# Kernel optimization log

Hardware: AMD Instinct MI355X
Metric: run time of the kernel (lower is better)

The kernel has to match this reference:

```python
import jax, jax.numpy as jnp
import numpy as np

B, Z, L = 256, 256, 8
C0, H0, W0 = 128, 8, 8
O = C0 * H0 * W0  # 8192


def _conv_transpose(x, w, b):
    """Torch ConvTranspose2d(k=4, s=2, p=1) equivalent.
    w: torch layout (in_ch, out_ch, kH, kW).
    Implemented as lhs-dilated conv with flipped, transposed kernel; pad = k-1-p = 2.
    """
    wt = jnp.flip(w, (2, 3)).transpose(1, 0, 2, 3)  # (out, in, kh, kw)
    y = jax.lax.conv_general_dilated(
        x, wt, window_strides=(1, 1), padding=[(2, 2), (2, 2)],
        lhs_dilation=(2, 2), dimension_numbers=('NCHW', 'OIHW', 'NCHW'))
    return y + b[None, :, None, None]


def setup_inputs() -> dict:
    key = jax.random.key(0)
    ks = jax.random.split(key, 6)
    return {
        'x': jax.random.normal(ks[0], (B, Z), jnp.float32),
        'gw': jax.random.normal(ks[1], (Z, L), jnp.float32) * (2.0 / (Z + L)) ** 0.5,  # xavier_normal
        'gb': jnp.zeros((L,), jnp.float32),
        'pw': jax.random.normal(ks[2], (O, Z, L), jnp.float32) * (1.0 / Z) ** 0.5,  # kaiming linear
        'pb': jnp.zeros((O, L), jnp.float32),
        'w1': jax.random.normal(ks[3], (C0, 64, 4, 4), jnp.float32) * 0.02,
        'b1': jnp.zeros((64,), jnp.float32),
        'w2': jax.random.normal(ks[4], (64, 32, 4, 4), jnp.float32) * 0.02,
        'b2': jnp.zeros((32,), jnp.float32),
        'w3': jax.random.normal(ks[5], (32, 3, 4, 4), jnp.float32) * 0.02,
        'b3': jnp.zeros((3,), jnp.float32),
    }


def reference(x, gw, gb, pw, pb, w1, b1, w2, b2, w3, b3):
    # --- ME mixture of linear experts (linear projection) ---
    g = jax.nn.softmax(x @ gw + gb, axis=1)               # (B, L)
    # Per-expert linear outputs, then gate-weighted sum. Mathematically equal to
    # torch's (pw @ gatings) per-sample weight followed by bmm with x, but avoids
    # the (B, O, Z) intermediate.
    expert_out = jnp.einsum('bi,oil->bol', x, pw)          # (B, O, L)
    out = jnp.einsum('bol,bl->bo', expert_out, g) + g @ pb.T  # (B, O)
    # --- conv-transpose decoder stack ---
    h = out.reshape(B, C0, H0, W0)
    h = jax.nn.relu(_conv_transpose(h, w1, b1))            # (B, 64, 16, 16)
    h = jax.nn.relu(_conv_transpose(h, w2, b2))            # (B, 32, 32, 32)
    h = _conv_transpose(h, w3, b3)                         # (B, 3, 64, 64)
    return h
```

## Files before the change

kernel.cpp:

```cpp
#include <hip/hip_runtime.h>

typedef __bf16 bf16;
typedef __bf16 bf16x8 __attribute__((ext_vector_type(8)));
typedef float f32x4 __attribute__((ext_vector_type(4)));

__device__ __forceinline__ f32x4 mfma16(bf16x8 a, bf16x8 b, f32x4 c) {
  return __builtin_amdgcn_mfma_f32_16x16x32_bf16(a, b, c, 0, 0, 0);
}

__device__ __forceinline__ void gload16(const void* g, void* l) {
  __builtin_amdgcn_global_load_lds(
      (const __attribute__((address_space(1))) void*)g,
      (__attribute__((address_space(3))) void*)(uint32_t)(size_t)l, 16, 0, 0);
}

__device__ __forceinline__ bf16x8 cvt8(float4 a, float4 b) {
  bf16x8 r;
  r[0] = (bf16)a.x; r[1] = (bf16)a.y; r[2] = (bf16)a.z; r[3] = (bf16)a.w;
  r[4] = (bf16)b.x; r[5] = (bf16)b.y; r[6] = (bf16)b.z; r[7] = (bf16)b.w;
  return r;
}

__global__ __launch_bounds__(256) void gating_kernel(
    const float* __restrict__ x, const float* __restrict__ gw,
    const float* __restrict__ gb, bf16* __restrict__ xgbP,
    float* __restrict__ gbuf) {
  const int b = blockIdx.x, tid = threadIdx.x;
  __shared__ float xs[256];
  __shared__ float gs[8];
  xs[tid] = x[b * 256 + tid];
  __syncthreads();
  if (tid < 8) {
    float acc = gb[tid];
    for (int i = 0; i < 256; ++i) acc += xs[i] * gw[i * 8 + tid];
    gs[tid] = acc;
  }
  __syncthreads();
  if (tid == 0) {
    float m = gs[0];
    for (int l = 1; l < 8; ++l) m = fmaxf(m, gs[l]);
    float s = 0.f, e[8];
    for (int l = 0; l < 8; ++l) { e[l] = expf(gs[l] - m); s += e[l]; }
    float inv = 1.f / s;
    for (int l = 0; l < 8; ++l) gs[l] = e[l] * inv;
  }
  __syncthreads();
  if (tid < 8) gbuf[b * 8 + tid] = gs[tid];
  float xv = xs[tid];
  bf16x8 r;
#pragma unroll
  for (int j = 0; j < 8; ++j) r[j] = (bf16)(xv * gs[j]);
  size_t off = (size_t)(b >> 4) * 65536 + (size_t)(tid >> 2) * 1024 +
               (size_t)(((tid & 3) * 16 + (b & 15)) * 16);
  *(bf16x8*)((char*)xgbP + off) = r;
}

template <int CIN, int COUT, int COUTP>
__device__ __forceinline__ void cw_one(const float* __restrict__ w,
                                       bf16* __restrict__ wp, int idx) {
  constexpr int K = 4 * CIN;
  int ic = idx & (CIN - 1);
  int t = (idx / CIN) & 3;
  int oc = (idx / K) % COUTP;
  int p = idx / (K * COUTP);
  bf16 v = (bf16)0.f;
  if (oc < COUT) {
    int py = p >> 1, px = p & 1, tyi = t >> 1, txi = t & 1;
    int ky = py == 0 ? (tyi ? 3 : 1) : (tyi ? 2 : 0);
    int kx = px == 0 ? (txi ? 3 : 1) : (txi ? 2 : 0);
    v = (bf16)w[((ic * COUT + oc) * 4 + ky) * 4 + kx];
  }
  wp[idx] = v;
}

__global__ __launch_bounds__(256) void convert_w_all(
    const float* __restrict__ w1, bf16* __restrict__ w1p,
    const float* __restrict__ w2, bf16* __restrict__ w2p,
    const float* __restrict__ w3, bf16* __restrict__ w3p) {
  int idx = blockIdx.x * 256 + threadIdx.x;
  if (idx < 131072) cw_one<128, 64, 64>(w1, w1p, idx);
  else if (idx < 163840) cw_one<64, 32, 32>(w2, w2p, idx - 131072);
  else if (idx < 172032) cw_one<32, 3, 16>(w3, w3p, idx - 163840);
}

template <int HP, int WP, int C>
__device__ __forceinline__ void bz_one(bf16* __restrict__ buf, int idx) {
  constexpr int NCELL = 2 * WP + 2 * (HP - 2);
  constexpr int C8 = C / 8;
  int c8 = idx % C8;
  int rem = idx / C8;
  int cell = rem % NCELL;
  int b = rem / NCELL;
  int y, x;
  if (cell < WP) { y = 0; x = cell; }
  else if (cell < 2 * WP) { y = HP - 1; x = cell - WP; }
  else { int r2 = cell - 2 * WP; y = 1 + (r2 >> 1); x = (r2 & 1) ? WP - 1 : 0; }
  bf16x8 z = {};
  *(bf16x8*)(buf + ((size_t)(b * HP + y) * WP + x) * C + c8 * 8) = z;
}

__global__ __launch_bounds__(256) void border_zero_all(
    bf16* __restrict__ h0t, bf16* __restrict__ h1, bf16* __restrict__ h2) {
  int idx = blockIdx.x * 256 + threadIdx.x;
  if (idx < 147456) bz_one<10, 10, 128>(h0t, idx);
  else if (idx < 286720) bz_one<18, 18, 64>(h1, idx - 147456);
  else if (idx < 421888) bz_one<34, 34, 32>(h2, idx - 286720);
}

__global__ __launch_bounds__(512) void me_gemm_kernel(
    const float* __restrict__ pw, const bf16* __restrict__ xgbP,
    const float* __restrict__ pb, const float* __restrict__ gbuf,
    bf16* __restrict__ h0t) {
  __shared__ char sA[131072];
  const int tid = threadIdx.x, wv = tid >> 6, l = tid & 63;
  const int lr = l & 15, lkg = l >> 4;
  const int M0 = blockIdx.x * 32;

#pragma unroll 4
  for (int it = 0; it < 16; ++it) {
    int g = it * 512 + tid;
    int kt = g >> 8, rem = g & 255;
    int row = rem >> 3, ig = rem & 7;
    const float* src = pw + (size_t)(M0 + row) * 2048 + kt * 64 + ig * 8;
    float4 v0 = *(const float4*)src;
    float4 v1 = *(const float4*)(src + 4);
    int L = kt * 4096 + row * 128 + ((ig * 16) ^ ((row & 7) << 4));
    *(bf16x8*)(sA + L) = cvt8(v0, v1);
  }
  __syncthreads();

  int aoff[2][2];
#pragma unroll
  for (int m = 0; m < 2; ++m)
#pragma unroll
    for (int ks = 0; ks < 2; ++ks)
      aoff[m][ks] = (m * 16 + lr) * 128 + (((ks * 4 + lkg) * 16) ^ ((lr & 7) << 4));

  const char* pB0 = (const char*)xgbP + (size_t)(2 * wv) * 65536 + l * 16;
  const char* pB1 = (const char*)xgbP + (size_t)(2 * wv + 1) * 65536 + l * 16;

  f32x4 acc[2][2] = {};
#pragma unroll 8
  for (int s = 0; s < 64; ++s) {
    const int kt = s >> 1, ks = s & 1;
    const char* base = sA + kt * 4096;
    bf16x8 a0 = *(const bf16x8*)(base + aoff[0][ks]);
    bf16x8 a1 = *(const bf16x8*)(base + aoff[1][ks]);
    bf16x8 b0 = *(const bf16x8*)(pB0 + s * 1024);
    bf16x8 b1 = *(const bf16x8*)(pB1 + s * 1024);
    acc[0][0] = mfma16(a0, b0, acc[0][0]);
    acc[0][1] = mfma16(a0, b1, acc[0][1]);
    acc[1][0] = mfma16(a1, b0, acc[1][0]);
    acc[1][1] = mfma16(a1, b1, acc[1][1]);
  }

  float4 g0[2], g1[2];
#pragma unroll
  for (int n = 0; n < 2; ++n) {
    int b = wv * 32 + n * 16 + lr;
    g0[n] = *(const float4*)(gbuf + b * 8);
    g1[n] = *(const float4*)(gbuf + b * 8 + 4);
  }
#pragma unroll
  for (int m = 0; m < 2; ++m)
#pragma unroll
    for (int r = 0; r < 4; ++r) {
      int o = M0 + m * 16 + lkg * 4 + r;
      float4 p0 = *(const float4*)(pb + o * 8);
      float4 p1 = *(const float4*)(pb + o * 8 + 4);
      int cch = o >> 6, y = (o >> 3) & 7, xx = o & 7;
#pragma unroll
      for (int n = 0; n < 2; ++n) {
        int b = wv * 32 + n * 16 + lr;
        float bias = g0[n].x * p0.x + g0[n].y * p0.y + g0[n].z * p0.z + g0[n].w * p0.w +
                     g1[n].x * p1.x + g1[n].y * p1.y + g1[n].z * p1.z + g1[n].w * p1.w;
        h0t[((size_t)(b * 10 + y + 1) * 10 + xx + 1) * 128 + cch] = (bf16)(acc[m][n][r] + bias);
      }
    }
}

template <int CIN, int H, int YB, int COUTP, int WM, int NF, int SWM,
          bool WLDS, int INIT, int WIT, bool RELU, bool F32OUT, int SIN_SZ, int SW_SZ>
__global__ __launch_bounds__(256) void convt_kernel(
    const bf16* __restrict__ in, const bf16* __restrict__ wp,
    const float* __restrict__ bias, bf16* __restrict__ out,
    float* __restrict__ fout) {
  constexpr int W = H, WROW = W + 2, ROWB = CIN * 2, GRS = ROWB / 16;
  constexpr int LGR = (GRS == 16) ? 4 : (GRS == 8) ? 3 : 2;
  constexpr int LW = (W == 8) ? 3 : (W == 16) ? 4 : 5;
  constexpr int K = 4 * CIN;
  constexpr int CHUNKS = (YB + 2) * WROW * GRS;
  constexpr int WGR = K / 8;
  __shared__ char sIn[SIN_SZ];
  __shared__ char sW[SW_SZ];

  const int tid = threadIdx.x, wv = tid >> 6, l = tid & 63;
  const int nyb = H / YB;
  const int img = blockIdx.x / nyb, y0 = (blockIdx.x % nyb) * YB;
  const int p = blockIdx.y, py = p >> 1, px = p & 1;

#pragma unroll
  for (int it = 0; it < INIT; ++it) {
    int t = it * 256 + tid;
    int tc = t < CHUNKS ? t : CHUNKS - 1;
    int pix = tc >> LGR, cc = tc & (GRS - 1);
    int ly = pix / WROW, lx = pix % WROW;
    int sb = (cc * 16) ^ ((pix & SWM) << 4);
    gload16(in + ((size_t)((img * (H + 2) + y0 + ly) * (W + 2) + lx)) * CIN + (sb >> 1),
            sIn + it * 4096 + wv * 1024);
  }
  if constexpr (WLDS) {
#pragma unroll
    for (int it = 0; it < WIT; ++it) {
      int t = it * 256 + tid;
      int oc = t / WGR, cc = t % WGR;
      int sb = (cc * 16) ^ ((oc & 7) << 4);
      gload16(wp + (size_t)(p * COUTP + oc) * K + (sb >> 1), sW + it * 4096 + wv * 1024);
    }
  }
  __syncthreads();

  const int lr = l & 15, lkg = l >> 4;
  const int wm = wv & (WM - 1), wn = wv / WM;
  int pcen[2];
#pragma unroll
  for (int m = 0; m < 2; ++m) {
    int r = wm * 32 + m * 16 + lr;
    pcen[m] = ((r >> LW) + 1) * WROW + (r & (W - 1)) + 1;
  }

  f32x4 acc[2][NF] = {};
#pragma unroll 4
  for (int kk = 0; kk < K; kk += 32) {
    const int t4 = kk / CIN;
    const int tyi = t4 >> 1, txi = t4 & 1;
    const int dy = (py == 0) ? (tyi ? -1 : 0) : (tyi ? 0 : 1);
    const int dx = (px == 0) ? (txi ? -1 : 0) : (txi ? 0 : 1);
    const int icb = (kk % CIN) * 2 + lkg * 16;
    bf16x8 av[2], bv[NF];
#pragma unroll
    for (int m = 0; m < 2; ++m) {
      int pixd = pcen[m] + dy * WROW + dx;
      av[m] = *(const bf16x8*)(sIn + pixd * ROWB + (icb ^ ((pixd & SWM) << 4)));
    }
#pragma unroll
    for (int n = 0; n < NF; ++n) {
      int oc = (wn * NF + n) * 16 + lr;
      if constexpr (WLDS) {
        int kb = kk * 2 + lkg * 16;
        bv[n] = *(const bf16x8*)(sW + oc * (K * 2) + (kb ^ ((oc & 7) << 4)));
      } else {
        bv[n] = *(const bf16x8*)(wp + (size_t)(p * COUTP + oc) * K + kk + lkg * 8);
      }
    }
#pragma unroll
    for (int m = 0; m < 2; ++m)
#pragma unroll
      for (int n = 0; n < NF; ++n) acc[m][n] = mfma16(av[m], bv[n], acc[m][n]);
  }

#pragma unroll
  for (int m = 0; m < 2; ++m)
#pragma unroll
    for (int r4 = 0; r4 < 4; ++r4) {
      int r = wm * 32 + m * 16 + lkg * 4 + r4;
      int yy = r >> LW, xx = r & (W - 1);
      int oy = 2 * (y0 + yy) + py, ox = 2 * xx + px;
#pragma unroll
      for (int n = 0; n < NF; ++n) {
        int oc = (wn * NF + n) * 16 + lr;
        float v = acc[m][n][r4];
        if constexpr (F32OUT) {
          if (oc < 3) fout[((size_t)(img * 3 + oc) * (2 * H) + oy) * (2 * H) + ox] = v + bias[oc];
        } else {
          v += bias[oc];
          if constexpr (RELU) v = fmaxf(v, 0.f);
          out[((size_t)(img * (2 * H + 2) + oy + 1) * (2 * H + 2) + ox + 1) * COUTP + oc] = (bf16)v;
        }
      }
    }
}

extern "C" void kernel_launch(void* const* d_in, const int* in_sizes, int n_in,
                              void* d_out, int out_size, void* d_ws, size_t ws_size,
                              hipStream_t stream) {
  const float* x  = (const float*)d_in[0];
  const float* gw = (const float*)d_in[1];
  const float* gb = (const float*)d_in[2];
  const float* pw = (const float*)d_in[3];
  const float* pb = (const float*)d_in[4];
  const float* w1 = (const float*)d_in[5];
  const float* b1 = (const float*)d_in[6];
  const float* w2 = (const float*)d_in[7];
  const float* b2 = (const float*)d_in[8];
  const float* w3 = (const float*)d_in[9];
  const float* b3 = (const float*)d_in[10];
  float* outp = (float*)d_out;

  char* ws = (char*)d_ws;
  bf16*  xgbP = (bf16*)(ws + 0);
  float* gbuf = (float*)(ws + 1048576);
  bf16*  h0t  = (bf16*)(ws + 1056768);
  bf16*  w1p  = (bf16*)(ws + 7610368);
  bf16*  h1   = (bf16*)(ws + 7872512);
  bf16*  w2p  = (bf16*)(ws + 18489344);
  bf16*  h2   = (bf16*)(ws + 18554880);
  bf16*  w3p  = (bf16*)(ws + 37494784);

  border_zero_all<<<1648, 256, 0, stream>>>(h0t, h1, h2);
  gating_kernel<<<256, 256, 0, stream>>>(x, gw, gb, xgbP, gbuf);
  convert_w_all<<<672, 256, 0, stream>>>(w1, w1p, w2, w2p, w3, w3p);

  me_gemm_kernel<<<256, 512, 0, stream>>>(pw, xgbP, pb, gbuf, h0t);

  convt_kernel<128, 8, 8, 64, 2, 2, 7, false, 7, 0, true, false, 28672, 16>
      <<<dim3(256, 4), 256, 0, stream>>>(h0t, w1p, b1, h1, nullptr);
  convt_kernel<64, 16, 8, 32, 4, 2, 7, true, 6, 4, true, false, 24576, 16384>
      <<<dim3(512, 4), 256, 0, stream>>>(h1, w2p, b2, h2, nullptr);
  convt_kernel<32, 32, 4, 16, 4, 1, 3, true, 4, 1, false, true, 16384, 4096>
      <<<dim3(2048, 4), 256, 0, stream>>>(h2, w3p, b3, nullptr, outp);
}
```

Measured before the change: 115.6 us.

## Fold four conv-transpose parities into one block and halve ME GEMM tile

Each conv-transpose block now loops over all four output parity classes itself, so the staged input tile in LDS is loaded once and reused four times instead of being reloaded by four separate grid-y blocks. Weight staging in LDS is dropped and weights are read straight from global memory. Separately, the ME GEMM tile shrinks from 32 to 16 rows, halving LDS use and doubling the block count. The trade-offs are four times the accumulator registers per thread, a quarter of the conv blocks, and more global weight traffic.

```diff
diff --git a/kernel.cpp b/kernel.cpp
--- a/kernel.cpp
+++ b/kernel.cpp
@@ -111,47 +111,42 @@
     const float* __restrict__ pw, const bf16* __restrict__ xgbP,
     const float* __restrict__ pb, const float* __restrict__ gbuf,
     bf16* __restrict__ h0t) {
-  __shared__ char sA[131072];
+  __shared__ char sA[65536];
   const int tid = threadIdx.x, wv = tid >> 6, l = tid & 63;
   const int lr = l & 15, lkg = l >> 4;
-  const int M0 = blockIdx.x * 32;
-
-#pragma unroll 4
-  for (int it = 0; it < 16; ++it) {
+  const int M0 = blockIdx.x * 16;
+
+#pragma unroll
+  for (int it = 0; it < 8; ++it) {
     int g = it * 512 + tid;
-    int kt = g >> 8, rem = g & 255;
+    int kt = g >> 7, rem = g & 127;
     int row = rem >> 3, ig = rem & 7;
     const float* src = pw + (size_t)(M0 + row) * 2048 + kt * 64 + ig * 8;
     float4 v0 = *(const float4*)src;
     float4 v1 = *(const float4*)(src + 4);
-    int L = kt * 4096 + row * 128 + ((ig * 16) ^ ((row & 7) << 4));
+    int L = kt * 2048 + row * 128 + ((ig * 16) ^ ((row & 7) << 4));
     *(bf16x8*)(sA + L) = cvt8(v0, v1);
   }
   __syncthreads();
 
-  int aoff[2][2];
-#pragma unroll
-  for (int m = 0; m < 2; ++m)
-#pragma unroll
-    for (int ks = 0; ks < 2; ++ks)
-      aoff[m][ks] = (m * 16 + lr) * 128 + (((ks * 4 + lkg) * 16) ^ ((lr & 7) << 4));
+  int aoff[2];
+#pragma unroll
+  for (int ks = 0; ks < 2; ++ks)
+    aoff[ks] = lr * 128 + (((ks * 4 + lkg) * 16) ^ ((lr & 7) << 4));
 
   const char* pB0 = (const char*)xgbP + (size_t)(2 * wv) * 65536 + l * 16;
   const char* pB1 = (const char*)xgbP + (size_t)(2 * wv + 1) * 65536 + l * 16;
 
-  f32x4 acc[2][2] = {};
+  f32x4 acc[2] = {};
 #pragma unroll 8
   for (int s = 0; s < 64; ++s) {
     const int kt = s >> 1, ks = s & 1;
-    const char* base = sA + kt * 4096;
-    bf16x8 a0 = *(const bf16x8*)(base + aoff[0][ks]);
-    bf16x8 a1 = *(const bf16x8*)(base + aoff[1][ks]);
+    const char* base = sA + kt * 2048;
+    bf16x8 a0 = *(const bf16x8*)(base + aoff[ks]);
     bf16x8 b0 = *(const bf16x8*)(pB0 + s * 1024);
     bf16x8 b1 = *(const bf16x8*)(pB1 + s * 1024);
-    acc[0][0] = mfma16(a0, b0, acc[0][0]);
-    acc[0][1] = mfma16(a0, b1, acc[0][1]);
-    acc[1][0] = mfma16(a1, b0, acc[1][0]);
-    acc[1][1] = mfma16(a1, b1, acc[1][1]);
+    acc[0] = mfma16(a0, b0, acc[0]);
+    acc[1] = mfma16(a0, b1, acc[1]);
   }
 
   float4 g0[2], g1[2];
@@ -162,25 +157,23 @@
     g1[n] = *(const float4*)(gbuf + b * 8 + 4);
   }
 #pragma unroll
-  for (int m = 0; m < 2; ++m)
-#pragma unroll
-    for (int r = 0; r < 4; ++r) {
-      int o = M0 + m * 16 + lkg * 4 + r;
-      float4 p0 = *(const float4*)(pb + o * 8);
-      float4 p1 = *(const float4*)(pb + o * 8 + 4);
-      int cch = o >> 6, y = (o >> 3) & 7, xx = o & 7;
-#pragma unroll
-      for (int n = 0; n < 2; ++n) {
-        int b = wv * 32 + n * 16 + lr;
-        float bias = g0[n].x * p0.x + g0[n].y * p0.y + g0[n].z * p0.z + g0[n].w * p0.w +
-                     g1[n].x * p1.x + g1[n].y * p1.y + g1[n].z * p1.z + g1[n].w * p1.w;
-        h0t[((size_t)(b * 10 + y + 1) * 10 + xx + 1) * 128 + cch] = (bf16)(acc[m][n][r] + bias);
-      }
+  for (int r = 0; r < 4; ++r) {
+    int o = M0 + lkg * 4 + r;
+    float4 p0 = *(const float4*)(pb + o * 8);
+    float4 p1 = *(const float4*)(pb + o * 8 + 4);
+    int cch = o >> 6, y = (o >> 3) & 7, xx = o & 7;
+#pragma unroll
+    for (int n = 0; n < 2; ++n) {
+      int b = wv * 32 + n * 16 + lr;
+      float bias = g0[n].x * p0.x + g0[n].y * p0.y + g0[n].z * p0.z + g0[n].w * p0.w +
+                   g1[n].x * p1.x + g1[n].y * p1.y + g1[n].z * p1.z + g1[n].w * p1.w;
+      h0t[((size_t)(b * 10 + y + 1) * 10 + xx + 1) * 128 + cch] = (bf16)(acc[n][r] + bias);
     }
-}
-
-template <int CIN, int H, int YB, int COUTP, int WM, int NF, int SWM,
-          bool WLDS, int INIT, int WIT, bool RELU, bool F32OUT, int SIN_SZ, int SW_SZ>
+  }
+}
+
+template <int CIN, int H, int YB, int COUTP, int WM, int NF, int SWM, int INIT,
+          bool RELU, bool F32OUT, int SIN_SZ>
 __global__ __launch_bounds__(256) void convt_kernel(
     const bf16* __restrict__ in, const bf16* __restrict__ wp,
     const float* __restrict__ bias, bf16* __restrict__ out,
@@ -190,14 +183,11 @@
   constexpr int LW = (W == 8) ? 3 : (W == 16) ? 4 : 5;
   constexpr int K = 4 * CIN;
   constexpr int CHUNKS = (YB + 2) * WROW * GRS;
-  constexpr int WGR = K / 8;
   __shared__ char sIn[SIN_SZ];
-  __shared__ char sW[SW_SZ];
 
   const int tid = threadIdx.x, wv = tid >> 6, l = tid & 63;
   const int nyb = H / YB;
   const int img = blockIdx.x / nyb, y0 = (blockIdx.x % nyb) * YB;
-  const int p = blockIdx.y, py = p >> 1, px = p & 1;
 
 #pragma unroll
   for (int it = 0; it < INIT; ++it) {
@@ -209,15 +199,6 @@
     gload16(in + ((size_t)((img * (H + 2) + y0 + ly) * (W + 2) + lx)) * CIN + (sb >> 1),
             sIn + it * 4096 + wv * 1024);
   }
-  if constexpr (WLDS) {
-#pragma unroll
-    for (int it = 0; it < WIT; ++it) {
-      int t = it * 256 + tid;
-      int oc = t / WGR, cc = t % WGR;
-      int sb = (cc * 16) ^ ((oc & 7) << 4);
-      gload16(wp + (size_t)(p * COUTP + oc) * K + (sb >> 1), sW + it * 4096 + wv * 1024);
-    }
-  }
   __syncthreads();
 
   const int lr = l & 15, lkg = l >> 4;
@@ -229,56 +210,59 @@
     pcen[m] = ((r >> LW) + 1) * WROW + (r & (W - 1)) + 1;
   }
 
-  f32x4 acc[2][NF] = {};
+  f32x4 acc[4][2][NF] = {};
+#pragma unroll
+  for (int p = 0; p < 4; ++p) {
+    const int py = p >> 1, px = p & 1;
 #pragma unroll 4
-  for (int kk = 0; kk < K; kk += 32) {
-    const int t4 = kk / CIN;
-    const int tyi = t4 >> 1, txi = t4 & 1;
-    const int dy = (py == 0) ? (tyi ? -1 : 0) : (tyi ? 0 : 1);
-    const int dx = (px == 0) ? (txi ? -1 : 0) : (txi ? 0 : 1);
-    const int icb = (kk % CIN) * 2 + lkg * 16;
-    bf16x8 av[2], bv[NF];
-#pragma unroll
-    for (int m = 0; m < 2; ++m) {
-      int pixd = pcen[m] + dy * WROW + dx;
-      av[m] = *(const bf16x8*)(sIn + pixd * ROWB + (icb ^ ((pixd & SWM) << 4)));
-    }
-#pragma unroll
-    for (int n = 0; n < NF; ++n) {
-      int oc = (wn * NF + n) * 16 + lr;
-      if constexpr (WLDS) {
-        int kb = kk * 2 + lkg * 16;
-        bv[n] = *(const bf16x8*)(sW + oc * (K * 2) + (kb ^ ((oc & 7) << 4)));
-      } else {
+    for (int kk = 0; kk < K; kk += 32) {
+      const int t4 = kk / CIN;
+      const int tyi = t4 >> 1, txi = t4 & 1;
+      const int dy = (py == 0) ? (tyi ? -1 : 0) : (tyi ? 0 : 1);
+      const int dx = (px == 0) ? (txi ? -1 : 0) : (txi ? 0 : 1);
+      const int icb = (kk % CIN) * 2 + lkg * 16;
+      bf16x8 av[2], bv[NF];
+#pragma unroll
+      for (int m = 0; m < 2; ++m) {
+        int pixd = pcen[m] + dy * WROW + dx;
+        av[m] = *(const bf16x8*)(sIn + pixd * ROWB + (icb ^ ((pixd & SWM) << 4)));
+      }
+#pragma unroll
+      for (int n = 0; n < NF; ++n) {
+        int oc = (wn * NF + n) * 16 + lr;
         bv[n] = *(const bf16x8*)(wp + (size_t)(p * COUTP + oc) * K + kk + lkg * 8);
       }
+#pragma unroll
+      for (int m = 0; m < 2; ++m)
+#pragma unroll
+        for (int n = 0; n < NF; ++n) acc[p][m][n] = mfma16(av[m], bv[n], acc[p][m][n]);
     }
+  }
+
+#pragma unroll
+  for (int p = 0; p < 4; ++p) {
+    const int py = p >> 1, px = p & 1;
 #pragma unroll
     for (int m = 0; m < 2; ++m)
 #pragma unroll
-      for (int n = 0; n < NF; ++n) acc[m][n] = mfma16(av[m], bv[n], acc[m][n]);
-  }
-
-#pragma unroll
-  for (int m = 0; m < 2; ++m)
-#pragma unroll
-    for (int r4 = 0; r4 < 4; ++r4) {
-      int r = wm * 32 + m * 16 + lkg * 4 + r4;
-      int yy = r >> LW, xx = r & (W - 1);
-      int oy = 2 * (y0 + yy) + py, ox = 2 * xx + px;
-#pragma unroll
-      for (int n = 0; n < NF; ++n) {
-        int oc = (wn * NF + n) * 16 + lr;
-        float v = acc[m][n][r4];
-        if constexpr (F32OUT) {
-          if (oc < 3) fout[((size_t)(img * 3 + oc) * (2 * H) + oy) * (2 * H) + ox] = v + bias[oc];
-        } else {
-          v += bias[oc];
-          if constexpr (RELU) v = fmaxf(v, 0.f);
-          out[((size_t)(img * (2 * H + 2) + oy + 1) * (2 * H + 2) + ox + 1) * COUTP + oc] = (bf16)v;
+      for (int r4 = 0; r4 < 4; ++r4) {
+        int r = wm * 32 + m * 16 + lkg * 4 + r4;
+        int yy = r >> LW, xx = r & (W - 1);
+        int oy = 2 * (y0 + yy) + py, ox = 2 * xx + px;
+#pragma unroll
+        for (int n = 0; n < NF; ++n) {
+          int oc = (wn * NF + n) * 16 + lr;
+          float v = acc[p][m][n][r4];
+          if constexpr (F32OUT) {
+            if (oc < 3) fout[((size_t)(img * 3 + oc) * (2 * H) + oy) * (2 * H) + ox] = v + bias[oc];
+          } else {
+            v += bias[oc];
+            if constexpr (RELU) v = fmaxf(v, 0.f);
+            out[((size_t)(img * (2 * H + 2) + oy + 1) * (2 * H + 2) + ox + 1) * COUTP + oc] = (bf16)v;
+          }
         }
       }
-    }
+  }
 }
 
 extern "C" void kernel_launch(void* const* d_in, const int* in_sizes, int n_in,
@@ -311,12 +295,12 @@
   gating_kernel<<<256, 256, 0, stream>>>(x, gw, gb, xgbP, gbuf);
   convert_w_all<<<672, 256, 0, stream>>>(w1, w1p, w2, w2p, w3, w3p);
 
-  me_gemm_kernel<<<256, 512, 0, stream>>>(pw, xgbP, pb, gbuf, h0t);
-
-  convt_kernel<128, 8, 8, 64, 2, 2, 7, false, 7, 0, true, false, 28672, 16>
-      <<<dim3(256, 4), 256, 0, stream>>>(h0t, w1p, b1, h1, nullptr);
-  convt_kernel<64, 16, 8, 32, 4, 2, 7, true, 6, 4, true, false, 24576, 16384>
-      <<<dim3(512, 4), 256, 0, stream>>>(h1, w2p, b2, h2, nullptr);
-  convt_kernel<32, 32, 4, 16, 4, 1, 3, true, 4, 1, false, true, 16384, 4096>
-      <<<dim3(2048, 4), 256, 0, stream>>>(h2, w3p, b3, nullptr, outp);
-}
+  me_gemm_kernel<<<512, 512, 0, stream>>>(pw, xgbP, pb, gbuf, h0t);
+
+  convt_kernel<128, 8, 8, 64, 2, 2, 7, 7, true, false, 28672>
+      <<<256, 256, 0, stream>>>(h0t, w1p, b1, h1, nullptr);
+  convt_kernel<64, 16, 8, 32, 4, 2, 7, 6, true, false, 24576>
+      <<<512, 256, 0, stream>>>(h1, w2p, b2, h2, nullptr);
+  convt_kernel<32, 32, 4, 16, 4, 1, 3, 4, false, true, 16384>
+      <<<2048, 256, 0, stream>>>(h2, w3p, b3, nullptr, outp);
+}
```

After: 124.5 us. 1.08x slower.

## Merge prep kernels into one launch and halve ME GEMM row tile

Applied to the files above, without the earlier changes.

The border-zeroing, gating/softmax and weight-conversion kernels are merged into a single prep kernel, with block-index ranges selecting each role, so two launches go away. The ME GEMM now covers 16 output rows per block instead of 32, which doubles the grid to 512 blocks and halves LDS use to 64KB. The aim is more occupancy and better spread across CUs on a memory-bound load of pw. In exchange, each block reloads the xgbP B operand for half as much compute, so B-operand traffic doubles.

```diff
diff --git a/kernel.cpp b/kernel.cpp
--- a/kernel.cpp
+++ b/kernel.cpp
@@ -19,40 +19,6 @@
   r[0] = (bf16)a.x; r[1] = (bf16)a.y; r[2] = (bf16)a.z; r[3] = (bf16)a.w;
   r[4] = (bf16)b.x; r[5] = (bf16)b.y; r[6] = (bf16)b.z; r[7] = (bf16)b.w;
   return r;
-}
-
-__global__ __launch_bounds__(256) void gating_kernel(
-    const float* __restrict__ x, const float* __restrict__ gw,
-    const float* __restrict__ gb, bf16* __restrict__ xgbP,
-    float* __restrict__ gbuf) {
-  const int b = blockIdx.x, tid = threadIdx.x;
-  __shared__ float xs[256];
-  __shared__ float gs[8];
-  xs[tid] = x[b * 256 + tid];
-  __syncthreads();
-  if (tid < 8) {
-    float acc = gb[tid];
-    for (int i = 0; i < 256; ++i) acc += xs[i] * gw[i * 8 + tid];
-    gs[tid] = acc;
-  }
-  __syncthreads();
-  if (tid == 0) {
-    float m = gs[0];
-    for (int l = 1; l < 8; ++l) m = fmaxf(m, gs[l]);
-    float s = 0.f, e[8];
-    for (int l = 0; l < 8; ++l) { e[l] = expf(gs[l] - m); s += e[l]; }
-    float inv = 1.f / s;
-    for (int l = 0; l < 8; ++l) gs[l] = e[l] * inv;
-  }
-  __syncthreads();
-  if (tid < 8) gbuf[b * 8 + tid] = gs[tid];
-  float xv = xs[tid];
-  bf16x8 r;
-#pragma unroll
-  for (int j = 0; j < 8; ++j) r[j] = (bf16)(xv * gs[j]);
-  size_t off = (size_t)(b >> 4) * 65536 + (size_t)(tid >> 2) * 1024 +
-               (size_t)(((tid & 3) * 16 + (b & 15)) * 16);
-  *(bf16x8*)((char*)xgbP + off) = r;
 }
 
 template <int CIN, int COUT, int COUTP>
@@ -73,16 +39,6 @@
   wp[idx] = v;
 }
 
-__global__ __launch_bounds__(256) void convert_w_all(
-    const float* __restrict__ w1, bf16* __restrict__ w1p,
-    const float* __restrict__ w2, bf16* __restrict__ w2p,
-    const float* __restrict__ w3, bf16* __restrict__ w3p) {
-  int idx = blockIdx.x * 256 + threadIdx.x;
-  if (idx < 131072) cw_one<128, 64, 64>(w1, w1p, idx);
-  else if (idx < 163840) cw_one<64, 32, 32>(w2, w2p, idx - 131072);
-  else if (idx < 172032) cw_one<32, 3, 16>(w3, w3p, idx - 163840);
-}
-
 template <int HP, int WP, int C>
 __device__ __forceinline__ void bz_one(bf16* __restrict__ buf, int idx) {
   constexpr int NCELL = 2 * WP + 2 * (HP - 2);
@@ -99,59 +55,97 @@
   *(bf16x8*)(buf + ((size_t)(b * HP + y) * WP + x) * C + c8 * 8) = z;
 }
 
-__global__ __launch_bounds__(256) void border_zero_all(
+__global__ __launch_bounds__(256) void prep_kernel(
+    const float* __restrict__ x, const float* __restrict__ gw,
+    const float* __restrict__ gb, bf16* __restrict__ xgbP,
+    float* __restrict__ gbuf,
+    const float* __restrict__ w1, bf16* __restrict__ w1p,
+    const float* __restrict__ w2, bf16* __restrict__ w2p,
+    const float* __restrict__ w3, bf16* __restrict__ w3p,
     bf16* __restrict__ h0t, bf16* __restrict__ h1, bf16* __restrict__ h2) {
-  int idx = blockIdx.x * 256 + threadIdx.x;
-  if (idx < 147456) bz_one<10, 10, 128>(h0t, idx);
-  else if (idx < 286720) bz_one<18, 18, 64>(h1, idx - 147456);
-  else if (idx < 421888) bz_one<34, 34, 32>(h2, idx - 286720);
+  __shared__ float xs[256];
+  __shared__ float gs[8];
+  const int bid = blockIdx.x, tid = threadIdx.x;
+  if (bid < 256) {
+    const int b = bid;
+    xs[tid] = x[b * 256 + tid];
+    __syncthreads();
+    if (tid < 8) {
+      float acc = gb[tid];
+      for (int i = 0; i < 256; ++i) acc += xs[i] * gw[i * 8 + tid];
+      gs[tid] = acc;
+    }
+    __syncthreads();
+    if (tid == 0) {
+      float m = gs[0];
+      for (int l = 1; l < 8; ++l) m = fmaxf(m, gs[l]);
+      float s = 0.f, e[8];
+      for (int l = 0; l < 8; ++l) { e[l] = expf(gs[l] - m); s += e[l]; }
+      float inv = 1.f / s;
+      for (int l = 0; l < 8; ++l) gs[l] = e[l] * inv;
+    }
+    __syncthreads();
+    if (tid < 8) gbuf[b * 8 + tid] = gs[tid];
+    float xv = xs[tid];
+    bf16x8 r;
+#pragma unroll
+    for (int j = 0; j < 8; ++j) r[j] = (bf16)(xv * gs[j]);
+    size_t off = (size_t)(b >> 4) * 65536 + (size_t)(tid >> 2) * 1024 +
+                 (size_t)(((tid & 3) * 16 + (b & 15)) * 16);
+    *(bf16x8*)((char*)xgbP + off) = r;
+  } else if (bid < 928) {
+    int idx = (bid - 256) * 256 + tid;
+    if (idx < 131072) cw_one<128, 64, 64>(w1, w1p, idx);
+    else if (idx < 163840) cw_one<64, 32, 32>(w2, w2p, idx - 131072);
+    else if (idx < 172032) cw_one<32, 3, 16>(w3, w3p, idx - 163840);
+  } else {
+    int idx = (bid - 928) * 256 + tid;
+    if (idx < 147456) bz_one<10, 10, 128>(h0t, idx);
+    else if (idx < 286720) bz_one<18, 18, 64>(h1, idx - 147456);
+    else if (idx < 421888) bz_one<34, 34, 32>(h2, idx - 286720);
+  }
 }
 
 __global__ __launch_bounds__(512) void me_gemm_kernel(
     const float* __restrict__ pw, const bf16* __restrict__ xgbP,
     const float* __restrict__ pb, const float* __restrict__ gbuf,
     bf16* __restrict__ h0t) {
-  __shared__ char sA[131072];
+  __shared__ char sA[65536];
   const int tid = threadIdx.x, wv = tid >> 6, l = tid & 63;
   const int lr = l & 15, lkg = l >> 4;
-  const int M0 = blockIdx.x * 32;
-
-#pragma unroll 4
-  for (int it = 0; it < 16; ++it) {
+  const int M0 = blockIdx.x * 16;
+
+#pragma unroll
+  for (int it = 0; it < 8; ++it) {
     int g = it * 512 + tid;
-    int kt = g >> 8, rem = g & 255;
+    int kt = g >> 7, rem = g & 127;
     int row = rem >> 3, ig = rem & 7;
     const float* src = pw + (size_t)(M0 + row) * 2048 + kt * 64 + ig * 8;
     float4 v0 = *(const float4*)src;
     float4 v1 = *(const float4*)(src + 4);
-    int L = kt * 4096 + row * 128 + ((ig * 16) ^ ((row & 7) << 4));
+    int L = kt * 2048 + row * 128 + ((ig * 16) ^ ((row & 7) << 4));
     *(bf16x8*)(sA + L) = cvt8(v0, v1);
   }
   __syncthreads();
 
-  int aoff[2][2];
-#pragma unroll
-  for (int m = 0; m < 2; ++m)
-#pragma unroll
-    for (int ks = 0; ks < 2; ++ks)
-      aoff[m][ks] = (m * 16 + lr) * 128 + (((ks * 4 + lkg) * 16) ^ ((lr & 7) << 4));
+  int aoff[2];
+#pragma unroll
+  for (int ks = 0; ks < 2; ++ks)
+    aoff[ks] = lr * 128 + (((ks * 4 + lkg) * 16) ^ ((lr & 7) << 4));
 
   const char* pB0 = (const char*)xgbP + (size_t)(2 * wv) * 65536 + l * 16;
   const char* pB1 = (const char*)xgbP + (size_t)(2 * wv + 1) * 65536 + l * 16;
 
-  f32x4 acc[2][2] = {};
+  f32x4 acc[2] = {};
 #pragma unroll 8
   for (int s = 0; s < 64; ++s) {
     const int kt = s >> 1, ks = s & 1;
-    const char* base = sA + kt * 4096;
-    bf16x8 a0 = *(const bf16x8*)(base + aoff[0][ks]);
-    bf16x8 a1 = *(const bf16x8*)(base + aoff[1][ks]);
+    const char* base = sA + kt * 2048;
+    bf16x8 a0 = *(const bf16x8*)(base + aoff[ks]);
     bf16x8 b0 = *(const bf16x8*)(pB0 + s * 1024);
     bf16x8 b1 = *(const bf16x8*)(pB1 + s * 1024);
-    acc[0][0] = mfma16(a0, b0, acc[0][0]);
-    acc[0][1] = mfma16(a0, b1, acc[0][1]);
-    acc[1][0] = mfma16(a1, b0, acc[1][0]);
-    acc[1][1] = mfma16(a1, b1, acc[1][1]);
+    acc[0] = mfma16(a0, b0, acc[0]);
+    acc[1] = mfma16(a0, b1, acc[1]);
   }
 
   float4 g0[2], g1[2];
@@ -162,21 +156,19 @@
     g1[n] = *(const float4*)(gbuf + b * 8 + 4);
   }
 #pragma unroll
-  for (int m = 0; m < 2; ++m)
-#pragma unroll
-    for (int r = 0; r < 4; ++r) {
-      int o = M0 + m * 16 + lkg * 4 + r;
-      float4 p0 = *(const float4*)(pb + o * 8);
-      float4 p1 = *(const float4*)(pb + o * 8 + 4);
-      int cch = o >> 6, y = (o >> 3) & 7, xx = o & 7;
-#pragma unroll
-      for (int n = 0; n < 2; ++n) {
-        int b = wv * 32 + n * 16 + lr;
-        float bias = g0[n].x * p0.x + g0[n].y * p0.y + g0[n].z * p0.z + g0[n].w * p0.w +
-                     g1[n].x * p1.x + g1[n].y * p1.y + g1[n].z * p1.z + g1[n].w * p1.w;
-        h0t[((size_t)(b * 10 + y + 1) * 10 + xx + 1) * 128 + cch] = (bf16)(acc[m][n][r] + bias);
-      }
-    }
+  for (int r = 0; r < 4; ++r) {
+    int o = M0 + lkg * 4 + r;
+    float4 p0 = *(const float4*)(pb + o * 8);
+    float4 p1 = *(const float4*)(pb + o * 8 + 4);
+    int cch = o >> 6, y = (o >> 3) & 7, xx = o & 7;
+#pragma unroll
+    for (int n = 0; n < 2; ++n) {
+      int b = wv * 32 + n * 16 + lr;
+      float bias = g0[n].x * p0.x + g0[n].y * p0.y + g0[n].z * p0.z + g0[n].w * p0.w +
+                   g1[n].x * p1.x + g1[n].y * p1.y + g1[n].z * p1.z + g1[n].w * p1.w;
+      h0t[((size_t)(b * 10 + y + 1) * 10 + xx + 1) * 128 + cch] = (bf16)(acc[n][r] + bias);
+    }
+  }
 }
 
 template <int CIN, int H, int YB, int COUTP, int WM, int NF, int SWM,
@@ -307,11 +299,10 @@
   bf16*  h2   = (bf16*)(ws + 18554880);
   bf16*  w3p  = (bf16*)(ws + 37494784);
 
-  border_zero_all<<<1648, 256, 0, stream>>>(h0t, h1, h2);
-  gating_kernel<<<256, 256, 0, stream>>>(x, gw, gb, xgbP, gbuf);
-  convert_w_all<<<672, 256, 0, stream>>>(w1, w1p, w2, w2p, w3, w3p);
-
-  me_gemm_kernel<<<256, 512, 0, stream>>>(pw, xgbP, pb, gbuf, h0t);
+  prep_kernel<<<2576, 256, 0, stream>>>(x, gw, gb, xgbP, gbuf,
+                                        w1, w1p, w2, w2p, w3, w3p, h0t, h1, h2);
+
+  me_gemm_kernel<<<512, 512, 0, stream>>>(pw, xgbP, pb, gbuf, h0t);
 
   convt_kernel<128, 8, 8, 64, 2, 2, 7, false, 7, 0, true, false, 28672, 16>
       <<<dim3(256, 4), 256, 0, stream>>>(h0t, w1p, b1, h1, nullptr);
```

Measured after the change: 100.9 us, median of 2. 12.7% less time.
